# Kernel tuning notes

Hardware: AMD Instinct MI355X
Metric: run time of the kernel (lower is better)

Reference implementation:

```python
import jax, jax.numpy as jnp
import numpy as np

EMBED_DIM = 1024
NUM_HEADS = 16
HEAD_DIM = EMBED_DIM // NUM_HEADS


def setup_inputs() -> dict:
    key = jax.random.key(0)
    ks = jax.random.split(key, 9)
    B, S, D = 2, 2048, EMBED_DIM
    scale = 1.0 / np.sqrt(D)
    x = jax.random.normal(ks[0], (B, S, D), dtype=jnp.float32)
    # Linear params (torch nn.Linear: y = x @ W.T + b); store W as [out, in]
    Wq = jax.random.normal(ks[1], (D, D), dtype=jnp.float32) * scale
    bq = jnp.zeros((D,), dtype=jnp.float32)
    Wk = jax.random.normal(ks[2], (D, D), dtype=jnp.float32) * scale
    bk = jnp.zeros((D,), dtype=jnp.float32)
    Wv = jax.random.normal(ks[3], (D, D), dtype=jnp.float32) * scale
    bv = jnp.zeros((D,), dtype=jnp.float32)
    Wo = jax.random.normal(ks[4], (D, D), dtype=jnp.float32) * scale
    bo = jnp.zeros((D,), dtype=jnp.float32)
    return {"x": x, "Wq": Wq, "bq": bq, "Wk": Wk, "bk": bk,
            "Wv": Wv, "bv": bv, "Wo": Wo, "bo": bo}


def reference(x, Wq, bq, Wk, bk, Wv, bv, Wo, bo):
    B, S, D = x.shape
    H, Hd = NUM_HEADS, HEAD_DIM
    scaling = Hd ** -0.5
    # projections (torch Linear: x @ W.T + b)
    q = (x @ Wq.T + bq).reshape(B, S, H, Hd).transpose(0, 2, 1, 3)  # [B,H,S,Hd]
    k = (x @ Wk.T + bk).reshape(B, S, H, Hd).transpose(0, 2, 1, 3)
    v = (x @ Wv.T + bv).reshape(B, S, H, Hd).transpose(0, 2, 1, 3)
    # full score matrix, as in the original (no flash tiling)
    scores = jnp.einsum('bhqd,bhkd->bhqk', q, k) * scaling  # [B,H,S,S]
    attn = jax.nn.softmax(scores, axis=-1)
    # dropout is identity in eval mode
    out = jnp.einsum('bhqk,bhkd->bhqd', attn, v)  # [B,H,S,Hd]
    out = out.transpose(0, 2, 1, 3).reshape(B, S, D)
    return out @ Wo.T + bo
```

## Files before the change

kernel.cpp:

```cpp
#include <hip/hip_runtime.h>
#include <stdint.h>

typedef unsigned short u16;
typedef short short8 __attribute__((ext_vector_type(8)));
typedef float f32x4 __attribute__((ext_vector_type(4)));
typedef float f32x16 __attribute__((ext_vector_type(16)));
typedef float f32x2 __attribute__((ext_vector_type(2)));

__device__ __forceinline__ u16 f2bf_fast(float f) {
  union { float f; uint32_t u; } x;
  x.f = f;
  return (u16)((x.u + 0x8000u) >> 16);
}

__device__ __forceinline__ uint32_t pack2bf(float lo, float hi) {
  union { float f; uint32_t u; } a, b;
  a.f = lo; b.f = hi;
  return __builtin_amdgcn_perm(b.u + 0x8000u, a.u + 0x8000u, 0x07060302u);
}

__device__ __forceinline__ float bf2f(uint32_t u) {
  union { uint32_t u; float f; } x;
  x.u = u << 16;
  return x.f;
}

__device__ __forceinline__ uint32_t cvtpk(float lo, float hi) {
  uint32_t r;
  asm("v_cvt_pk_bf16_f32 %0, %1, %2" : "=v"(r) : "v"(lo), "v"(hi));
  return r;
}

__device__ __forceinline__ void permswap(uint32_t& a, uint32_t& b) {
  asm("v_permlane32_swap_b32 %0, %1" : "+v"(a), "+v"(b));
}

__device__ __forceinline__ void gload_lds16(const void* g, void* l) {
  __builtin_amdgcn_global_load_lds(
      (const __attribute__((address_space(1))) void*)g,
      (__attribute__((address_space(3))) void*)l, 16, 0, 0);
}

__device__ __forceinline__ f32x4 mfma16(short8 a, short8 b, f32x4 c) {
  return __builtin_amdgcn_mfma_f32_16x16x32_bf16(a, b, c, 0, 0, 0);
}

__device__ __forceinline__ f32x16 mfma32(short8 a, short8 b, f32x16 c) {
  return __builtin_amdgcn_mfma_f32_32x32x16_bf16(a, b, c, 0, 0, 0);
}

#define QSCALE 0.18033688011112042f

__global__ void pack_all(const float* __restrict__ x, const float* __restrict__ wq,
                         const float* __restrict__ wk, const float* __restrict__ wv,
                         const float* __restrict__ wo, u16* __restrict__ xp,
                         u16* __restrict__ wp) {
  const int gi = blockIdx.x * 256 + threadIdx.x;
  const int lane = gi & 63;
  const int kc = (gi >> 6) & 31;
  const int rt = gi >> 11;
  const int col = kc * 32 + (lane >> 4) * 8;
  const float* src;
  int row;
  if (rt < 256) {
    src = x;
    row = rt * 16 + (lane & 15);
  } else {
    const int wti = rt - 256;
    const int widx = wti >> 6;
    src = (widx == 0) ? wq : (widx == 1) ? wk : (widx == 2) ? wv : wo;
    row = (wti & 63) * 16 + (lane & 15);
  }
  const float4* p = (const float4*)(src + (size_t)row * 1024 + col);
  const float4 v0 = p[0], v1 = p[1];
  uint4 o;
  o.x = pack2bf(v0.x, v0.y);
  o.y = pack2bf(v0.z, v0.w);
  o.z = pack2bf(v1.x, v1.y);
  o.w = pack2bf(v1.z, v1.w);
  u16* dst = (rt < 256) ? xp : wp;
  const int og = (rt < 256) ? gi : gi - 524288;
  ((uint4*)dst)[og] = o;
}

__global__ __launch_bounds__(256, 3) void proj_qkv(
    const u16* __restrict__ xp, const u16* __restrict__ wp,
    const float* __restrict__ bq, const float* __restrict__ bk,
    const float* __restrict__ bv, u16* __restrict__ qw, u16* __restrict__ kw,
    u16* __restrict__ vw) {
  __shared__ __align__(16) u16 As[12288];
  __shared__ __align__(16) u16 Bs[12288];
  const int tid = threadIdx.x, lane = tid & 63, w = tid >> 6;
  const int quad = lane >> 4, l15 = lane & 15;

  const int bid = blockIdx.x;
  const int work = (bid & 7) * 96 + (bid >> 3);
  const bool isQK = work < 512;
  int at0, bt0, bm2, bn2;
  const u16 *Ap, *Bp;
  if (isQK) {
    bm2 = work >> 4; bn2 = work & 15;
    Ap = xp; at0 = bm2 * 8;
    Bp = wp; bt0 = bn2 * 8;
  } else {
    const int h = work - 512;
    bm2 = h >> 5; bn2 = h & 31;
    Ap = wp; at0 = 128 + bm2 * 8;
    Bp = xp; bt0 = bn2 * 8;
  }
  const int wr = w >> 1, wc = w & 1;
  const int bm = bm2 * 2 + wr, bn = bn2 * 2 + wc;

  auto stage = [&](int kc, int buf) {
#pragma unroll
    for (int i = 0; i < 4; ++i) {
      const int g = w * 4 + i;
      const int t = g & 7;
      const u16* src = (g < 8)
          ? (Ap + (((at0 + t) << 5) + kc) * 512 + lane * 8)
          : (Bp + (((bt0 + t) << 5) + kc) * 512 + lane * 8);
      u16* dst = ((g < 8) ? As : Bs) + (buf * 8 + t) * 512 + lane * 8;
      gload_lds16(src, dst);
    }
  };

  f32x4 acc[4][4] = {};

  stage(0, 0);
  stage(1, 1);

#pragma unroll
  for (int kc = 0; kc < 32; ++kc) {
    if (kc < 31)
      asm volatile("s_waitcnt vmcnt(4)" ::: "memory");
    else
      asm volatile("s_waitcnt vmcnt(0)" ::: "memory");
    __builtin_amdgcn_s_barrier();
    if (kc < 30) stage(kc + 2, (kc + 2) % 3);

    const u16* Ab = As + (kc % 3) * 4096;
    const u16* Bb = Bs + (kc % 3) * 4096;
    short8 af[4], bf[4];
#pragma unroll
    for (int mt = 0; mt < 4; ++mt)
      af[mt] = *(const short8*)&Ab[((wr * 4 + mt) * 64 + lane) * 8];
#pragma unroll
    for (int nt = 0; nt < 4; ++nt)
      bf[nt] = *(const short8*)&Bb[((wc * 4 + nt) * 64 + lane) * 8];

#pragma unroll
    for (int mt = 0; mt < 4; ++mt)
#pragma unroll
      for (int nt = 0; nt < 4; ++nt)
        acc[mt][nt] = mfma16(af[mt], bf[nt], acc[mt][nt]);
  }

#pragma unroll
  for (int nt = 0; nt < 4; ++nt) {
    const int n = bn * 64 + nt * 16 + l15;
#pragma unroll
    for (int mt = 0; mt < 4; ++mt)
#pragma unroll
      for (int r = 0; r < 4; ++r) {
        const int m = bm * 64 + mt * 16 + quad * 4 + r;
        const float a = acc[mt][nt][r];
        if (isQK) {
          const bool isQ = (bn < 16);
          const int nn = isQ ? n : n - 1024;
          const float v = isQ ? (a + bq[nn]) * QSCALE : a + bk[nn];
          u16* op = isQ ? qw : kw;
          const int b = m >> 11, s = m & 2047, hh = nn >> 6, d = nn & 63;
          op[((size_t)((b * 16 + hh) * 2048 + s)) * 64 + d] = f2bf_fast(v);
        } else {
          const float v = a + bv[m];
          const int b = n >> 11, s = n & 2047;
          vw[((size_t)(b * 1024 + m)) * 2048 + s] = f2bf_fast(v);
        }
      }
  }
}

__global__ __launch_bounds__(512, 4) void attn_kernel(
    const u16* __restrict__ Q, const u16* __restrict__ Kt,
    const u16* __restrict__ Vt, u16* __restrict__ awp) {
  __shared__ __align__(16) u16 Sm[40960];
  const int tid = threadIdx.x, lane = tid & 63, w = tid >> 6;
  const int l31 = lane & 31, hi = lane >> 5, l7 = lane & 7;
  const int kh = w >> 2, qg = w & 3;
  const int qt = blockIdx.x;
  const int bh = blockIdx.y;

  const char* Qb = (const char*)(Q + ((size_t)bh * 2048 + qt * 128) * 64);
  const char* Kb = (const char*)(Kt + (size_t)bh * 2048 * 64);
  const char* Vb = (const char*)(Vt + (size_t)bh * 64 * 2048);

  auto stageKV = [&](int j, int buf) {
#pragma unroll
    for (int h = 0; h < 2; ++h) {
      const int kt = h * 16 + j;
      u16* Kl = Sm + (buf * 2 + h) * 8192;
      u16* Vl = Kl + 4096;
      const int G = w * 64 + lane;
      const int r = G >> 3, sl = G & 7;
      gload_lds16(Kb + (size_t)(kt * 64 + r) * 128 + ((sl ^ (r & 7)) * 16),
                  &Kl[G * 8]);
      gload_lds16(Vb + (size_t)r * 4096 + kt * 128 + ((sl ^ (r & 7)) * 16),
                  &Vl[G * 8]);
    }
  };

  u16* Qs = Sm + 32768;
#pragma unroll
  for (int i = 0; i < 2; ++i) {
    const int G = (w * 2 + i) * 64 + lane;
    const int row = G >> 3, sl = G & 7;
    gload_lds16(Qb + (size_t)row * 128 + ((sl ^ (row & 7)) * 16), &Qs[G * 8]);
  }
  stageKV(0, 0);
  __syncthreads();

  short8 aq[4];
#pragma unroll
  for (int ds = 0; ds < 4; ++ds)
    aq[ds] = *(const short8*)&Qs[(qg * 32 + l31) * 64 + (((ds << 1) + hi) ^ l7) * 8];

  f32x16 ot[2] = {};
  f32x2 l2 = {0.f, 0.f};

  for (int j = 0; j < 16; ++j) {
    const int buf = j & 1;
    if (j < 15) stageKV(j + 1, buf ^ 1);
    const u16* Kl = Sm + (buf * 2 + kh) * 8192;
    const u16* Vl = Kl + 4096;

    f32x16 st[2];
    __builtin_amdgcn_s_setprio(1);
#pragma unroll
    for (int t = 0; t < 2; ++t) {
      f32x16 s = {};
#pragma unroll
      for (int ds = 0; ds < 4; ++ds) {
        short8 kf = *(const short8*)&Kl[(t * 32 + l31) * 64 +
                                        (((ds << 1) + hi) ^ l7) * 8];
        s = mfma32(kf, aq[ds], s);
      }
      st[t] = s;
    }
    __builtin_amdgcn_s_setprio(0);

    union { uint32_t u[4]; short8 s; } pb[2][2];
#pragma unroll
    for (int t = 0; t < 2; ++t) {
      float e[16];
#pragma unroll
      for (int i = 0; i < 16; ++i) e[i] = __builtin_amdgcn_exp2f(st[t][i]);
#pragma unroll
      for (int i = 0; i < 8; ++i) l2 += (f32x2){e[2 * i], e[2 * i + 1]};
      uint32_t p01 = cvtpk(e[0], e[1]),   p23 = cvtpk(e[2], e[3]);
      uint32_t p45 = cvtpk(e[4], e[5]),   p67 = cvtpk(e[6], e[7]);
      uint32_t p89 = cvtpk(e[8], e[9]),   pAB = cvtpk(e[10], e[11]);
      uint32_t pCD = cvtpk(e[12], e[13]), pEF = cvtpk(e[14], e[15]);
      permswap(p01, p45);
      permswap(p23, p67);
      permswap(p89, pCD);
      permswap(pAB, pEF);
      pb[t][0].u[0] = p01; pb[t][0].u[1] = p23; pb[t][0].u[2] = p45; pb[t][0].u[3] = p67;
      pb[t][1].u[0] = p89; pb[t][1].u[1] = pAB; pb[t][1].u[2] = pCD; pb[t][1].u[3] = pEF;
    }

    __builtin_amdgcn_s_setprio(1);
#pragma unroll
    for (int t = 0; t < 2; ++t)
#pragma unroll
      for (int dt = 0; dt < 2; ++dt)
#pragma unroll
        for (int s2 = 0; s2 < 2; ++s2) {
          short8 vf = *(const short8*)&Vl[(dt * 32 + l31) * 64 +
                                          ((((t * 2 + s2) << 1) + hi) ^ l7) * 8];
          ot[dt] = mfma32(vf, pb[t][s2].s, ot[dt]);
        }
    __builtin_amdgcn_s_setprio(0);

    if (j < 15) __syncthreads();
  }

  float l = l2.x + l2.y;
  l += __shfl_xor(l, 32);

  __syncthreads();
  float* fb = (float*)Sm;
  if (kh == 1) {
    float* p = fb + (qg * 64 + lane) * 34;
#pragma unroll
    for (int i = 0; i < 8; ++i) {
      *(f32x2*)(p + 2 * i)      = (f32x2){ot[0][2 * i], ot[0][2 * i + 1]};
      *(f32x2*)(p + 16 + 2 * i) = (f32x2){ot[1][2 * i], ot[1][2 * i + 1]};
    }
    p[32] = l;
  }
  __syncthreads();
  if (kh == 0) {
    const float* p = fb + (qg * 64 + lane) * 34;
#pragma unroll
    for (int i = 0; i < 16; ++i) ot[0][i] += p[i];
#pragma unroll
    for (int i = 0; i < 16; ++i) ot[1][i] += p[16 + i];
    l += p[32];
    const float inv = __builtin_amdgcn_rcpf(l);

    const int b = bh >> 4, h = bh & 15;
    const int rt = b * 128 + qt * 8 + qg * 2 + (l31 >> 4);
#pragma unroll
    for (int dt = 0; dt < 2; ++dt) {
      const int kc = h * 2 + dt;
#pragma unroll
      for (int g = 0; g < 4; ++g) {
        const int ln = (lane & 15) + 16 * g;
        uint2 ov;
        ov.x = cvtpk(ot[dt][4 * g + 0] * inv, ot[dt][4 * g + 1] * inv);
        ov.y = cvtpk(ot[dt][4 * g + 2] * inv, ot[dt][4 * g + 3] * inv);
        *(uint2*)(awp + ((size_t)((rt * 32 + kc) * 64 + ln)) * 8 + hi * 4) = ov;
      }
    }
  }
}

__global__ __launch_bounds__(512, 2) void out_proj(const u16* __restrict__ awp,
                                                   const u16* __restrict__ wp,
                                                   const float* __restrict__ bo,
                                                   float* __restrict__ out) {
  __shared__ __align__(16) u16 As[12288];
  __shared__ __align__(16) u16 Bs[12288];
  const int tid = threadIdx.x, lane = tid & 63, w = tid >> 6;
  const int quad = lane >> 4, l15 = lane & 15;

  const int bid = blockIdx.x;
  const int work = (bid & 7) * 32 + (bid >> 3);
  const int bm2 = work >> 3, bn2 = work & 7;
  const int at0 = bm2 * 8, bt0 = 192 + bn2 * 8;
  const int wr = w >> 2, wc = w & 3;

  auto stage = [&](int kc, int buf) {
#pragma unroll
    for (int i = 0; i < 2; ++i) {
      const int g = w * 2 + i;
      const int t = g & 7;
      const u16* src = (g < 8)
          ? (awp + (((at0 + t) << 5) + kc) * 512 + lane * 8)
          : (wp + (((bt0 + t) << 5) + kc) * 512 + lane * 8);
      u16* dst = ((g < 8) ? As : Bs) + (buf * 8 + t) * 512 + lane * 8;
      gload_lds16(src, dst);
    }
  };

  f32x4 acc[4][2] = {};

  stage(0, 0);
  stage(1, 1);

#pragma unroll
  for (int kc = 0; kc < 32; ++kc) {
    if (kc < 31)
      asm volatile("s_waitcnt vmcnt(2)" ::: "memory");
    else
      asm volatile("s_waitcnt vmcnt(0)" ::: "memory");
    __builtin_amdgcn_s_barrier();
    if (kc < 30) stage(kc + 2, (kc + 2) % 3);

    const u16* Ab = As + (kc % 3) * 4096;
    const u16* Bb = Bs + (kc % 3) * 4096;
    short8 af[4], bf[2];
#pragma unroll
    for (int mt = 0; mt < 4; ++mt)
      af[mt] = *(const short8*)&Ab[((wr * 4 + mt) * 64 + lane) * 8];
#pragma unroll
    for (int nt = 0; nt < 2; ++nt)
      bf[nt] = *(const short8*)&Bb[((wc * 2 + nt) * 64 + lane) * 8];

#pragma unroll
    for (int mt = 0; mt < 4; ++mt)
#pragma unroll
      for (int nt = 0; nt < 2; ++nt)
        acc[mt][nt] = mfma16(af[mt], bf[nt], acc[mt][nt]);
  }

#pragma unroll
  for (int nt = 0; nt < 2; ++nt) {
    const int n = bn2 * 128 + wc * 32 + nt * 16 + l15;
    const float bb = bo[n];
#pragma unroll
    for (int mt = 0; mt < 4; ++mt)
#pragma unroll
      for (int r = 0; r < 4; ++r) {
        const int m = bm2 * 128 + wr * 64 + mt * 16 + quad * 4 + r;
        out[(size_t)m * 1024 + n] = acc[mt][nt][r] + bb;
      }
  }
}

extern "C" void kernel_launch(void* const* d_in, const int* in_sizes, int n_in,
                              void* d_out, int out_size, void* d_ws, size_t ws_size,
                              hipStream_t stream) {
  const float* x  = (const float*)d_in[0];
  const float* Wq = (const float*)d_in[1];
  const float* bq = (const float*)d_in[2];
  const float* Wk = (const float*)d_in[3];
  const float* bk = (const float*)d_in[4];
  const float* Wv = (const float*)d_in[5];
  const float* bv = (const float*)d_in[6];
  const float* Wo = (const float*)d_in[7];
  const float* bo = (const float*)d_in[8];

  const size_t M4 = (size_t)4 * 1024 * 1024;
  u16* xp  = (u16*)d_ws;
  u16* wp  = xp + M4;
  u16* qw  = wp + M4;
  u16* kw  = qw + M4;
  u16* vw  = kw + M4;
  u16* awp = vw + M4;

  pack_all<<<4096, 256, 0, stream>>>(x, Wq, Wk, Wv, Wo, xp, wp);

  proj_qkv<<<768, 256, 0, stream>>>(xp, wp, bq, bk, bv, qw, kw, vw);

  attn_kernel<<<dim3(16, 32), 512, 0, stream>>>(qw, kw, vw, awp);

  out_proj<<<256, 512, 0, stream>>>(awp, wp, bo, (float*)d_out);
}
```

Before: 181.8 us.

## Triple-buffer smaller K/V tiles with vmcnt waits and load Q directly to registers

The attention kernel now streams K/V in 32-key chunks through a three-slot LDS ring. Each iteration prefetches two chunks ahead and waits with explicit vmcnt counts plus a raw barrier, replacing the previous double buffer of 64-key tiles with a full __syncthreads per step. Q fragments are loaded straight from global memory into registers instead of being staged through LDS. LDS use drops from 80 KB to 48 KB and the launch-bounds occupancy hint rises from 4 to 6, aiming to hide memory latency and fit more blocks per CU. The cost is twice as many loop iterations and barriers, plus uncoalesced global Q loads.

Measured after the change: 237.4 us. +30.6%, slower.

```diff
diff --git a/kernel.cpp b/kernel.cpp
--- a/kernel.cpp
+++ b/kernel.cpp
@@ -180,12 +180,12 @@
   }
 }
 
-__global__ __launch_bounds__(512, 4) void attn_kernel(
+__global__ __launch_bounds__(512, 6) void attn_kernel(
     const u16* __restrict__ Q, const u16* __restrict__ Kt,
     const u16* __restrict__ Vt, u16* __restrict__ awp) {
-  __shared__ __align__(16) u16 Sm[40960];
+  __shared__ __align__(16) u16 Sm[24576];
   const int tid = threadIdx.x, lane = tid & 63, w = tid >> 6;
-  const int l31 = lane & 31, hi = lane >> 5, l7 = lane & 7;
+  const int l31 = lane & 31, hi = lane >> 5, l7 = lane & 7, l3 = lane & 3;
   const int kh = w >> 2, qg = w & 3;
   const int qt = blockIdx.x;
   const int bh = blockIdx.y;
@@ -194,94 +194,91 @@
   const char* Kb = (const char*)(Kt + (size_t)bh * 2048 * 64);
   const char* Vb = (const char*)(Vt + (size_t)bh * 64 * 2048);
 
-  auto stageKV = [&](int j, int buf) {
-#pragma unroll
-    for (int h = 0; h < 2; ++h) {
-      const int kt = h * 16 + j;
-      u16* Kl = Sm + (buf * 2 + h) * 8192;
-      u16* Vl = Kl + 4096;
-      const int G = w * 64 + lane;
-      const int r = G >> 3, sl = G & 7;
-      gload_lds16(Kb + (size_t)(kt * 64 + r) * 128 + ((sl ^ (r & 7)) * 16),
-                  &Kl[G * 8]);
-      gload_lds16(Vb + (size_t)r * 4096 + kt * 128 + ((sl ^ (r & 7)) * 16),
-                  &Vl[G * 8]);
+  short8 aq[4];
+  const int qrow = qg * 32 + l31;
+#pragma unroll
+  for (int ds = 0; ds < 4; ++ds)
+    aq[ds] = *(const short8*)(Qb + (size_t)qrow * 128 + ds * 32 + hi * 16);
+
+  auto stageKV = [&](int j, int bs) {
+#pragma unroll
+    for (int i = 0; i < 2; ++i) {
+      const int G2 = i * 512 + tid;
+      const int h = G2 >> 9;
+      const int kv = (G2 >> 8) & 1;
+      const int g = G2 & 255;
+      u16* dst = Sm + (bs * 2 + h) * 4096 + kv * 2048 + g * 8;
+      if (kv == 0) {
+        const int r = g >> 3, sl = g & 7;
+        gload_lds16(Kb + (size_t)((h * 32 + j) * 32 + r) * 128 +
+                        ((sl ^ (r & 7)) * 16),
+                    dst);
+      } else {
+        const int r = g >> 2, sl = g & 3;
+        gload_lds16(Vb + (size_t)r * 4096 + (h * 32 + j) * 64 +
+                        ((sl ^ (r & 3)) * 16),
+                    dst);
+      }
     }
   };
 
-  u16* Qs = Sm + 32768;
-#pragma unroll
-  for (int i = 0; i < 2; ++i) {
-    const int G = (w * 2 + i) * 64 + lane;
-    const int row = G >> 3, sl = G & 7;
-    gload_lds16(Qb + (size_t)row * 128 + ((sl ^ (row & 7)) * 16), &Qs[G * 8]);
-  }
   stageKV(0, 0);
-  __syncthreads();
-
-  short8 aq[4];
-#pragma unroll
-  for (int ds = 0; ds < 4; ++ds)
-    aq[ds] = *(const short8*)&Qs[(qg * 32 + l31) * 64 + (((ds << 1) + hi) ^ l7) * 8];
+  stageKV(1, 1);
 
   f32x16 ot[2] = {};
   f32x2 l2 = {0.f, 0.f};
 
-  for (int j = 0; j < 16; ++j) {
-    const int buf = j & 1;
-    if (j < 15) stageKV(j + 1, buf ^ 1);
-    const u16* Kl = Sm + (buf * 2 + kh) * 8192;
-    const u16* Vl = Kl + 4096;
-
-    f32x16 st[2];
+  int bc = 0, bs = 2;
+  for (int j = 0; j < 32; ++j) {
+    if (j < 31)
+      asm volatile("s_waitcnt vmcnt(2)" ::: "memory");
+    else
+      asm volatile("s_waitcnt vmcnt(0)" ::: "memory");
+    __builtin_amdgcn_s_barrier();
+    if (j < 30) stageKV(j + 2, bs);
+
+    const u16* Kl = Sm + (bc * 2 + kh) * 4096;
+    const u16* Vl = Kl + 2048;
+
+    f32x16 st = {};
     __builtin_amdgcn_s_setprio(1);
 #pragma unroll
-    for (int t = 0; t < 2; ++t) {
-      f32x16 s = {};
-#pragma unroll
-      for (int ds = 0; ds < 4; ++ds) {
-        short8 kf = *(const short8*)&Kl[(t * 32 + l31) * 64 +
-                                        (((ds << 1) + hi) ^ l7) * 8];
-        s = mfma32(kf, aq[ds], s);
+    for (int ds = 0; ds < 4; ++ds) {
+      short8 kf = *(const short8*)&Kl[l31 * 64 + (((ds << 1) + hi) ^ l7) * 8];
+      st = mfma32(kf, aq[ds], st);
+    }
+    __builtin_amdgcn_s_setprio(0);
+
+    float e[16];
+#pragma unroll
+    for (int i = 0; i < 16; ++i) e[i] = __builtin_amdgcn_exp2f(st[i]);
+#pragma unroll
+    for (int i = 0; i < 8; ++i) l2 += (f32x2){e[2 * i], e[2 * i + 1]};
+    uint32_t p01 = cvtpk(e[0], e[1]),   p23 = cvtpk(e[2], e[3]);
+    uint32_t p45 = cvtpk(e[4], e[5]),   p67 = cvtpk(e[6], e[7]);
+    uint32_t p89 = cvtpk(e[8], e[9]),   pAB = cvtpk(e[10], e[11]);
+    uint32_t pCD = cvtpk(e[12], e[13]), pEF = cvtpk(e[14], e[15]);
+    permswap(p01, p45);
+    permswap(p23, p67);
+    permswap(p89, pCD);
+    permswap(pAB, pEF);
+    union { uint32_t u[4]; short8 s; } b0, b1;
+    b0.u[0] = p01; b0.u[1] = p23; b0.u[2] = p45; b0.u[3] = p67;
+    b1.u[0] = p89; b1.u[1] = pAB; b1.u[2] = pCD; b1.u[3] = pEF;
+
+    __builtin_amdgcn_s_setprio(1);
+#pragma unroll
+    for (int dt = 0; dt < 2; ++dt)
+#pragma unroll
+      for (int s2 = 0; s2 < 2; ++s2) {
+        short8 vf = *(const short8*)&Vl[(dt * 32 + l31) * 32 +
+                                        (((s2 * 2 + hi) ^ l3) * 8)];
+        ot[dt] = mfma32(vf, s2 ? b1.s : b0.s, ot[dt]);
       }
-      st[t] = s;
-    }
     __builtin_amdgcn_s_setprio(0);
 
-    union { uint32_t u[4]; short8 s; } pb[2][2];
-#pragma unroll
-    for (int t = 0; t < 2; ++t) {
-      float e[16];
-#pragma unroll
-      for (int i = 0; i < 16; ++i) e[i] = __builtin_amdgcn_exp2f(st[t][i]);
-#pragma unroll
-      for (int i = 0; i < 8; ++i) l2 += (f32x2){e[2 * i], e[2 * i + 1]};
-      uint32_t p01 = cvtpk(e[0], e[1]),   p23 = cvtpk(e[2], e[3]);
-      uint32_t p45 = cvtpk(e[4], e[5]),   p67 = cvtpk(e[6], e[7]);
-      uint32_t p89 = cvtpk(e[8], e[9]),   pAB = cvtpk(e[10], e[11]);
-      uint32_t pCD = cvtpk(e[12], e[13]), pEF = cvtpk(e[14], e[15]);
-      permswap(p01, p45);
-      permswap(p23, p67);
-      permswap(p89, pCD);
-      permswap(pAB, pEF);
-      pb[t][0].u[0] = p01; pb[t][0].u[1] = p23; pb[t][0].u[2] = p45; pb[t][0].u[3] = p67;
-      pb[t][1].u[0] = p89; pb[t][1].u[1] = pAB; pb[t][1].u[2] = pCD; pb[t][1].u[3] = pEF;
-    }
-
-    __builtin_amdgcn_s_setprio(1);
-#pragma unroll
-    for (int t = 0; t < 2; ++t)
-#pragma unroll
-      for (int dt = 0; dt < 2; ++dt)
-#pragma unroll
-        for (int s2 = 0; s2 < 2; ++s2) {
-          short8 vf = *(const short8*)&Vl[(dt * 32 + l31) * 64 +
-                                          ((((t * 2 + s2) << 1) + hi) ^ l7) * 8];
-          ot[dt] = mfma32(vf, pb[t][s2].s, ot[dt]);
-        }
-    __builtin_amdgcn_s_setprio(0);
-
-    if (j < 15) __syncthreads();
+    bc = (bc == 2) ? 0 : bc + 1;
+    bs = (bs == 2) ? 0 : bs + 1;
   }
 
   float l = l2.x + l2.y;
```
